# Performance work log

Hardware: AMD Instinct MI355X
Metric: run time of the kernel (lower is better)

The kernel has to match this reference:

```python
import jax, jax.numpy as jnp
import numpy as np

ITERS = 3
EPS = 1e-6


def setup_inputs() -> dict:
    key = jax.random.key(0)
    k1, k2 = jax.random.split(key, 2)
    a = jax.random.normal(k1, (64, 1152, 1, 1, 1, 1), dtype=jnp.float32)
    v = jax.random.normal(k2, (64, 1152, 32, 4, 4, 1), dtype=jnp.float32)
    logits = jnp.ones((1, 1152, 32, 1, 1, 1), dtype=jnp.float32)
    return {"a": a, "v": v, "logits": logits}


def _squash(s):
    # s: (batch, 1, B, P, P, 1); norm over dim 2 (matches torch code, dim=2)
    norm_sq = jnp.sum(s * s, axis=2, keepdims=True)
    return jnp.sqrt(norm_sq + EPS) / (1.0 + norm_sq) * s


def reference(a, v, logits):
    # a: (batch, A, 1, 1, 1, 1) -- unused (overwritten in original forward)
    # v: (batch, A, B, P, P, 1); logits: (1, A, B, 1, 1, 1)
    batch = v.shape[0]
    b = jnp.broadcast_to(logits, (batch,) + logits.shape[1:])
    p = None
    for i in range(ITERS):
        c = jax.nn.softmax(b, axis=2)                    # route over B
        s = jnp.sum(c * v, axis=1, keepdims=True)        # (batch,1,B,P,P,1)
        p = _squash(s)
        if i < ITERS - 1:
            # agreement: sum over pose dims -> (batch, A, B, 1, 1, 1)
            b = b + jnp.sum(p * v, axis=(-3, -2, -1), keepdims=True)
    p = jnp.squeeze(p, axis=1)                           # (batch, B, P, P, 1)
    a_out = jnp.linalg.norm(p, ord=2, axis=2)            # (batch, B, P, 1)
    return (a_out, p)
```

## Files before the change

kernel.cpp:

```cpp
#include <hip/hip_runtime.h>
#include <math.h>

#define BATCH 64
#define ADIM  1152
#define BDIM  32
#define SLICE 512
#define CHUNKS 16
#define ROWS  72
#define RPW   18
#define EPSQ  1e-6f
#define SPART_ITER ((size_t)BATCH * CHUNKS * SLICE)

typedef float v4f __attribute__((ext_vector_type(4)));


__device__ __forceinline__ void squash_from(const float* sp, int lane,
                                            v4f& sA, v4f& sB, v4f& fac) {
    const v4f* spv = (const v4f*)sp;
    sA = (v4f){0.f, 0.f, 0.f, 0.f};
    sB = (v4f){0.f, 0.f, 0.f, 0.f};
#pragma unroll
    for (int c = 0; c < CHUNKS; ++c) {
        sA += spv[c * 128 + lane];
        sB += spv[c * 128 + 64 + lane];
    }
    v4f nq = sA * sA + sB * sB;
#pragma unroll
    for (int off = 4; off <= 32; off <<= 1) {
        nq.x += __shfl_xor(nq.x, off, 64);
        nq.y += __shfl_xor(nq.y, off, 64);
        nq.z += __shfl_xor(nq.z, off, 64);
        nq.w += __shfl_xor(nq.w, off, 64);
    }
    fac.x = sqrtf(nq.x + EPSQ) / (1.f + nq.x);
    fac.y = sqrtf(nq.y + EPSQ) / (1.f + nq.y);
    fac.z = sqrtf(nq.z + EPSQ) / (1.f + nq.z);
    fac.w = sqrtf(nq.w + EPSQ) / (1.f + nq.w);
}

__device__ __forceinline__ void reduce_write(v4f* red, int lane, int wv,
                                             v4f ra, v4f rb, float* dst) {
    __syncthreads();
    if (wv == 3) { red[lane] = ra; red[64 + lane] = rb; }
    __syncthreads();
    if (wv == 2) { red[lane] += ra; red[64 + lane] += rb; }
    __syncthreads();
    if (wv == 1) { red[lane] += ra; red[64 + lane] += rb; }
    __syncthreads();
    if (wv == 0) {
        v4f* sp = (v4f*)dst;
        sp[lane]      = red[lane] + ra;
        sp[64 + lane] = red[64 + lane] + rb;
    }
}

__global__ __launch_bounds__(256) void pass0(
    const float* __restrict__ v,
    const float* __restrict__ logits,
    float* __restrict__ s0)
{
    const int bt    = blockIdx.x >> 4;
    const int chunk = blockIdx.x & 15;
    const int t     = threadIdx.x;
    const int lane  = t & 63;
    const int wv    = t >> 6;
    const int bq    = lane >> 2;
    const int a0    = chunk * ROWS;
    const int r0    = wv * RPW;

    __shared__ float w_sh[ROWS * BDIM];
    __shared__ v4f   red[128];

    if (t < ROWS) {
        const float* lr = logits + (size_t)(a0 + t) * BDIM;
        float e[BDIM];
        float s = 0.f;
#pragma unroll
        for (int b = 0; b < BDIM; ++b) { e[b] = __expf(lr[b]); s += e[b]; }
        float rd = 1.f / s;
#pragma unroll
        for (int b = 0; b < BDIM; ++b) w_sh[t * BDIM + b] = e[b] * rd;
    }
    __syncthreads();

    const v4f* vg = (const v4f*)(v + ((size_t)bt * ADIM + a0 + r0) * SLICE);
    v4f acc0 = (v4f){0.f, 0.f, 0.f, 0.f};
    v4f acc1 = (v4f){0.f, 0.f, 0.f, 0.f};

    v4f fA[6], fB[6];
#pragma unroll
    for (int u = 0; u < 6; ++u) fA[u] = vg[lane + 64 * u];

#pragma unroll
    for (int kk = 0; kk < 6; ++kk) {
        v4f* cur = (kk & 1) ? fB : fA;
        v4f* nxt = (kk & 1) ? fA : fB;
        if (kk + 1 < 6) {
#pragma unroll
            for (int u = 0; u < 6; ++u)
                nxt[u] = vg[lane + 64 * ((kk + 1) * 6 + u)];
        }
#pragma unroll
        for (int u = 0; u < 6; ++u) {
            const int j  = kk * 6 + u;
            const int rw = r0 + (j >> 1);
            if ((j & 1) == 0) acc0 += w_sh[rw * BDIM + bq] * cur[u];
            else              acc1 += w_sh[rw * BDIM + 16 + bq] * cur[u];
        }
    }

    reduce_write(red, lane, wv, acc0, acc1,
                 s0 + ((size_t)bt * CHUNKS + chunk) * SLICE);
}

__global__ __launch_bounds__(256) void iter_pass(
    const float* __restrict__ v,
    const float* __restrict__ logits,
    const float* __restrict__ s_part,
    float* __restrict__ s_next,
    int nprev)
{
    const int bt    = blockIdx.x >> 4;
    const int chunk = blockIdx.x & 15;
    const int t     = threadIdx.x;
    const int lane  = t & 63;
    const int wv    = t >> 6;
    const int bq    = lane >> 2;
    const int a0    = chunk * ROWS;
    const int r0    = wv * RPW;

    __shared__ v4f red[128];

    v4f pA = (v4f){0.f, 0.f, 0.f, 0.f};
    v4f pB = (v4f){0.f, 0.f, 0.f, 0.f};
    for (int j = 0; j < nprev; ++j) {
        v4f sA, sB, fac;
        squash_from(s_part + (size_t)j * SPART_ITER +
                    (size_t)bt * CHUNKS * SLICE, lane, sA, sB, fac);
        pA += fac * sA;
        pB += fac * sB;
    }

    const v4f*  vr  = (const v4f*)(v + ((size_t)bt * ADIM + a0 + r0) * SLICE);
    const float* lgr = logits + (size_t)(a0 + r0) * BDIM;

    v4f acc0 = (v4f){0.f, 0.f, 0.f, 0.f};
    v4f acc1 = (v4f){0.f, 0.f, 0.f, 0.f};

    v4f  vaN = vr[lane], vbN = vr[64 + lane];
    float b0N = lgr[bq], b1N = lgr[16 + bq];
#pragma unroll
    for (int r = 0; r < RPW; ++r) {
        v4f  va = vaN, vb = vbN;
        float b0 = b0N, b1 = b1N;
        if (r + 1 < RPW) {
            vaN = vr[(r + 1) * 128 + lane];
            vbN = vr[(r + 1) * 128 + 64 + lane];
            b0N = lgr[(r + 1) * BDIM + bq];
            b1N = lgr[(r + 1) * BDIM + 16 + bq];
        }
        float d0 = pA.x * va.x + pA.y * va.y + pA.z * va.z + pA.w * va.w;
        float d1 = pB.x * vb.x + pB.y * vb.y + pB.z * vb.z + pB.w * vb.w;
        d0 += __shfl_xor(d0, 1, 64); d0 += __shfl_xor(d0, 2, 64);
        d1 += __shfl_xor(d1, 1, 64); d1 += __shfl_xor(d1, 2, 64);
        float e0 = __expf(b0 + d0);
        float e1 = __expf(b1 + d1);
        float uu = e0 + e1;
#pragma unroll
        for (int off = 4; off <= 32; off <<= 1)
            uu += __shfl_xor(uu, off, 64);
        float rdc = __builtin_amdgcn_rcpf(uu);
        acc0 += (e0 * rdc) * va;
        acc1 += (e1 * rdc) * vb;
    }

    reduce_write(red, lane, wv, acc0, acc1,
                 s_next + ((size_t)bt * CHUNKS + chunk) * SLICE);
}

__global__ __launch_bounds__(512) void final_out(
    const float* __restrict__ s_part2,
    float* __restrict__ out)
{
    const int bt = blockIdx.x;
    const int t  = threadIdx.x;
    const int pose = t & 15;

    __shared__ float sq[SLICE];
    __shared__ float ns[16];

    float sv = 0.f;
#pragma unroll
    for (int c = 0; c < CHUNKS; ++c)
        sv += s_part2[((size_t)bt * CHUNKS + c) * SLICE + t];

    sq[t] = sv * sv;
    __syncthreads();
    if (t < 16) {
        float a = 0.f;
        for (int b2 = 0; b2 < BDIM; ++b2) a += sq[b2 * 16 + t];
        ns[t] = a;
    }
    __syncthreads();
    float n = ns[pose];
    float pv = sqrtf(n + EPSQ) / (1.f + n) * sv;

    out[8192 + (size_t)bt * SLICE + t] = pv;
    sq[t] = pv * pv;
    __syncthreads();
    if (t < 128) {
        const int b2 = t >> 2, p2 = t & 3;
        float a = 0.f;
#pragma unroll
        for (int p1 = 0; p1 < 4; ++p1) a += sq[b2 * 16 + p1 * 4 + p2];
        out[(size_t)bt * 128 + t] = sqrtf(a);
    }
}

extern "C" void kernel_launch(void* const* d_in, const int* in_sizes, int n_in,
                              void* d_out, int out_size, void* d_ws, size_t ws_size,
                              hipStream_t stream) {
    const float* v      = (const float*)d_in[1];
    const float* logits = (const float*)d_in[2];
    float* out    = (float*)d_out;
    float* s_part = (float*)d_ws;

    pass0<<<dim3(BATCH * CHUNKS), dim3(256), 0, stream>>>(
        v, logits, s_part);
    iter_pass<<<dim3(BATCH * CHUNKS), dim3(256), 0, stream>>>(
        v, logits, s_part, s_part + 1 * SPART_ITER, 1);
    iter_pass<<<dim3(BATCH * CHUNKS), dim3(256), 0, stream>>>(
        v, logits, s_part, s_part + 2 * SPART_ITER, 2);
    final_out<<<dim3(BATCH), dim3(512), 0, stream>>>(
        s_part + 2 * SPART_ITER, out);
}
```

Before: 272.2 us.

## Fuse all routing iterations into one persistent kernel with per-batch grid barriers

Replaces the four separate launches (pass0, two iter_pass, final_out) with a single kernel. Each batch's 8 chunk blocks synchronise through atomic counters in global memory, and the final squash and norm outputs are computed by chunk 0. Chunks are halved so each block covers 144 rows, and logits are cached in shared memory for reuse across iterations. This removes launch gaps and the separate final kernel. The cost is spin-wait barriers that require all 512 blocks to be co-resident to avoid deadlock, plus lower parallelism per batch.

```diff
diff --git a/kernel.cpp b/kernel.cpp
--- a/kernel.cpp
+++ b/kernel.cpp
@@ -5,9 +5,9 @@
 #define ADIM  1152
 #define BDIM  32
 #define SLICE 512
-#define CHUNKS 16
-#define ROWS  72
-#define RPW   18
+#define CHUNKS 8
+#define ROWS  144
+#define RPW   36
 #define EPSQ  1e-6f
 #define SPART_ITER ((size_t)BATCH * CHUNKS * SLICE)
 
@@ -54,13 +54,80 @@
     }
 }
 
-__global__ __launch_bounds__(256) void pass0(
+__device__ __forceinline__ void bar_release(unsigned* c) {
+    __threadfence();
+    __syncthreads();
+    if (threadIdx.x == 0)
+        __hip_atomic_fetch_add(c, 1u, __ATOMIC_RELEASE,
+                               __HIP_MEMORY_SCOPE_AGENT);
+}
+
+__device__ __forceinline__ void bar_wait(unsigned* c, unsigned target) {
+    if (threadIdx.x == 0) {
+        while (__hip_atomic_load(c, __ATOMIC_RELAXED,
+                                 __HIP_MEMORY_SCOPE_AGENT) < target)
+            __builtin_amdgcn_s_sleep(2);
+        (void)__hip_atomic_load(c, __ATOMIC_ACQUIRE,
+                                __HIP_MEMORY_SCOPE_AGENT);
+    }
+    __syncthreads();
+    __threadfence();
+}
+
+__device__ __forceinline__ void iter_sweep(const v4f* vw, const float* lg,
+                                           int lane, int bq, int r0,
+                                           v4f pA, v4f pB,
+                                           v4f& acc0, v4f& acc1) {
+    acc0 = (v4f){0.f, 0.f, 0.f, 0.f};
+    acc1 = (v4f){0.f, 0.f, 0.f, 0.f};
+    v4f fA[6], fB[6];
+#pragma unroll
+    for (int u = 0; u < 6; ++u) fA[u] = vw[lane + 64 * u];
+#pragma unroll 2
+    for (int g = 0; g < 12; ++g) {
+        v4f* cur = (g & 1) ? fB : fA;
+        v4f* nxt = (g & 1) ? fA : fB;
+        if (g + 1 < 12) {
+#pragma unroll
+            for (int u = 0; u < 6; ++u)
+                nxt[u] = vw[lane + 64 * ((g + 1) * 6 + u)];
+        }
+#pragma unroll
+        for (int i = 0; i < 3; ++i) {
+            const int rw = r0 + 3 * g + i;
+            v4f va = cur[2 * i], vb = cur[2 * i + 1];
+            float b0 = lg[rw * BDIM + bq];
+            float b1 = lg[rw * BDIM + 16 + bq];
+            float d0 = pA.x * va.x + pA.y * va.y + pA.z * va.z + pA.w * va.w;
+            float d1 = pB.x * vb.x + pB.y * vb.y + pB.z * vb.z + pB.w * vb.w;
+            d0 += __shfl_xor(d0, 1, 64); d0 += __shfl_xor(d0, 2, 64);
+            d1 += __shfl_xor(d1, 1, 64); d1 += __shfl_xor(d1, 2, 64);
+            float e0 = __expf(b0 + d0);
+            float e1 = __expf(b1 + d1);
+            float uu = e0 + e1;
+#pragma unroll
+            for (int off = 4; off <= 32; off <<= 1)
+                uu += __shfl_xor(uu, off, 64);
+            float rdc = __builtin_amdgcn_rcpf(uu);
+            acc0 += (e0 * rdc) * va;
+            acc1 += (e1 * rdc) * vb;
+        }
+    }
+}
+
+__global__ void zero_cnt(unsigned* cnt) {
+    if (threadIdx.x < BATCH) cnt[threadIdx.x] = 0u;
+}
+
+__global__ __launch_bounds__(256, 4) void route_all(
     const float* __restrict__ v,
     const float* __restrict__ logits,
-    float* __restrict__ s0)
+    float* s_part,
+    unsigned* cnt,
+    float* __restrict__ out)
 {
-    const int bt    = blockIdx.x >> 4;
-    const int chunk = blockIdx.x & 15;
+    const int bt    = blockIdx.x >> 3;
+    const int chunk = blockIdx.x & 7;
     const int t     = threadIdx.x;
     const int lane  = t & 63;
     const int wv    = t >> 6;
@@ -68,6 +135,7 @@
     const int a0    = chunk * ROWS;
     const int r0    = wv * RPW;
 
+    __shared__ float lg_sh[ROWS * BDIM];
     __shared__ float w_sh[ROWS * BDIM];
     __shared__ v4f   red[128];
 
@@ -76,144 +144,100 @@
         float e[BDIM];
         float s = 0.f;
 #pragma unroll
-        for (int b = 0; b < BDIM; ++b) { e[b] = __expf(lr[b]); s += e[b]; }
+        for (int b = 0; b < BDIM; ++b) {
+            float x = lr[b];
+            lg_sh[t * BDIM + b] = x;
+            e[b] = __expf(x);
+            s += e[b];
+        }
         float rd = 1.f / s;
 #pragma unroll
         for (int b = 0; b < BDIM; ++b) w_sh[t * BDIM + b] = e[b] * rd;
     }
     __syncthreads();
 
-    const v4f* vg = (const v4f*)(v + ((size_t)bt * ADIM + a0 + r0) * SLICE);
+    const v4f* vw = (const v4f*)(v + ((size_t)bt * ADIM + a0 + r0) * SLICE);
+    unsigned* cb = cnt + bt;
+
     v4f acc0 = (v4f){0.f, 0.f, 0.f, 0.f};
     v4f acc1 = (v4f){0.f, 0.f, 0.f, 0.f};
-
-    v4f fA[6], fB[6];
-#pragma unroll
-    for (int u = 0; u < 6; ++u) fA[u] = vg[lane + 64 * u];
-
-#pragma unroll
-    for (int kk = 0; kk < 6; ++kk) {
-        v4f* cur = (kk & 1) ? fB : fA;
-        v4f* nxt = (kk & 1) ? fA : fB;
-        if (kk + 1 < 6) {
-#pragma unroll
-            for (int u = 0; u < 6; ++u)
-                nxt[u] = vg[lane + 64 * ((kk + 1) * 6 + u)];
-        }
-#pragma unroll
-        for (int u = 0; u < 6; ++u) {
-            const int j  = kk * 6 + u;
-            const int rw = r0 + (j >> 1);
-            if ((j & 1) == 0) acc0 += w_sh[rw * BDIM + bq] * cur[u];
-            else              acc1 += w_sh[rw * BDIM + 16 + bq] * cur[u];
-        }
-    }
-
+    {
+        v4f fA[6], fB[6];
+#pragma unroll
+        for (int u = 0; u < 6; ++u) fA[u] = vw[lane + 64 * u];
+#pragma unroll 2
+        for (int kk = 0; kk < 12; ++kk) {
+            v4f* cur = (kk & 1) ? fB : fA;
+            v4f* nxt = (kk & 1) ? fA : fB;
+            if (kk + 1 < 12) {
+#pragma unroll
+                for (int u = 0; u < 6; ++u)
+                    nxt[u] = vw[lane + 64 * ((kk + 1) * 6 + u)];
+            }
+#pragma unroll
+            for (int u = 0; u < 6; ++u) {
+                const int j  = kk * 6 + u;
+                const int rw = r0 + (j >> 1);
+                if ((j & 1) == 0) acc0 += w_sh[rw * BDIM + bq] * cur[u];
+                else              acc1 += w_sh[rw * BDIM + 16 + bq] * cur[u];
+            }
+        }
+    }
     reduce_write(red, lane, wv, acc0, acc1,
-                 s0 + ((size_t)bt * CHUNKS + chunk) * SLICE);
-}
-
-__global__ __launch_bounds__(256) void iter_pass(
-    const float* __restrict__ v,
-    const float* __restrict__ logits,
-    const float* __restrict__ s_part,
-    float* __restrict__ s_next,
-    int nprev)
-{
-    const int bt    = blockIdx.x >> 4;
-    const int chunk = blockIdx.x & 15;
-    const int t     = threadIdx.x;
-    const int lane  = t & 63;
-    const int wv    = t >> 6;
-    const int bq    = lane >> 2;
-    const int a0    = chunk * ROWS;
-    const int r0    = wv * RPW;
-
-    __shared__ v4f red[128];
-
-    v4f pA = (v4f){0.f, 0.f, 0.f, 0.f};
-    v4f pB = (v4f){0.f, 0.f, 0.f, 0.f};
-    for (int j = 0; j < nprev; ++j) {
-        v4f sA, sB, fac;
-        squash_from(s_part + (size_t)j * SPART_ITER +
-                    (size_t)bt * CHUNKS * SLICE, lane, sA, sB, fac);
-        pA += fac * sA;
-        pB += fac * sB;
-    }
-
-    const v4f*  vr  = (const v4f*)(v + ((size_t)bt * ADIM + a0 + r0) * SLICE);
-    const float* lgr = logits + (size_t)(a0 + r0) * BDIM;
-
-    v4f acc0 = (v4f){0.f, 0.f, 0.f, 0.f};
-    v4f acc1 = (v4f){0.f, 0.f, 0.f, 0.f};
-
-    v4f  vaN = vr[lane], vbN = vr[64 + lane];
-    float b0N = lgr[bq], b1N = lgr[16 + bq];
-#pragma unroll
-    for (int r = 0; r < RPW; ++r) {
-        v4f  va = vaN, vb = vbN;
-        float b0 = b0N, b1 = b1N;
-        if (r + 1 < RPW) {
-            vaN = vr[(r + 1) * 128 + lane];
-            vbN = vr[(r + 1) * 128 + 64 + lane];
-            b0N = lgr[(r + 1) * BDIM + bq];
-            b1N = lgr[(r + 1) * BDIM + 16 + bq];
-        }
-        float d0 = pA.x * va.x + pA.y * va.y + pA.z * va.z + pA.w * va.w;
-        float d1 = pB.x * vb.x + pB.y * vb.y + pB.z * vb.z + pB.w * vb.w;
-        d0 += __shfl_xor(d0, 1, 64); d0 += __shfl_xor(d0, 2, 64);
-        d1 += __shfl_xor(d1, 1, 64); d1 += __shfl_xor(d1, 2, 64);
-        float e0 = __expf(b0 + d0);
-        float e1 = __expf(b1 + d1);
-        float uu = e0 + e1;
-#pragma unroll
-        for (int off = 4; off <= 32; off <<= 1)
-            uu += __shfl_xor(uu, off, 64);
-        float rdc = __builtin_amdgcn_rcpf(uu);
-        acc0 += (e0 * rdc) * va;
-        acc1 += (e1 * rdc) * vb;
-    }
-
+                 s_part + ((size_t)bt * CHUNKS + chunk) * SLICE);
+    bar_release(cb);
+    bar_wait(cb, 8);
+
+    v4f sA, sB, fac;
+    squash_from(s_part + (size_t)bt * CHUNKS * SLICE, lane, sA, sB, fac);
+    v4f pA = fac * sA;
+    v4f pB = fac * sB;
+
+    iter_sweep(vw, lg_sh, lane, bq, r0, pA, pB, acc0, acc1);
     reduce_write(red, lane, wv, acc0, acc1,
-                 s_next + ((size_t)bt * CHUNKS + chunk) * SLICE);
-}
-
-__global__ __launch_bounds__(512) void final_out(
-    const float* __restrict__ s_part2,
-    float* __restrict__ out)
-{
-    const int bt = blockIdx.x;
-    const int t  = threadIdx.x;
-    const int pose = t & 15;
-
-    __shared__ float sq[SLICE];
-    __shared__ float ns[16];
-
-    float sv = 0.f;
-#pragma unroll
-    for (int c = 0; c < CHUNKS; ++c)
-        sv += s_part2[((size_t)bt * CHUNKS + c) * SLICE + t];
-
-    sq[t] = sv * sv;
-    __syncthreads();
-    if (t < 16) {
-        float a = 0.f;
-        for (int b2 = 0; b2 < BDIM; ++b2) a += sq[b2 * 16 + t];
-        ns[t] = a;
-    }
-    __syncthreads();
-    float n = ns[pose];
-    float pv = sqrtf(n + EPSQ) / (1.f + n) * sv;
-
-    out[8192 + (size_t)bt * SLICE + t] = pv;
-    sq[t] = pv * pv;
-    __syncthreads();
-    if (t < 128) {
-        const int b2 = t >> 2, p2 = t & 3;
-        float a = 0.f;
-#pragma unroll
-        for (int p1 = 0; p1 < 4; ++p1) a += sq[b2 * 16 + p1 * 4 + p2];
-        out[(size_t)bt * 128 + t] = sqrtf(a);
+                 s_part + SPART_ITER + ((size_t)bt * CHUNKS + chunk) * SLICE);
+    bar_release(cb);
+    bar_wait(cb, 16);
+
+    squash_from(s_part + SPART_ITER + (size_t)bt * CHUNKS * SLICE,
+                lane, sA, sB, fac);
+    pA += fac * sA;
+    pB += fac * sB;
+
+    iter_sweep(vw, lg_sh, lane, bq, r0, pA, pB, acc0, acc1);
+    reduce_write(red, lane, wv, acc0, acc1,
+                 s_part + 2 * SPART_ITER + ((size_t)bt * CHUNKS + chunk) * SLICE);
+    bar_release(cb);
+
+    if (chunk != 0) return;
+    bar_wait(cb, 24);
+    if (wv != 0) return;
+
+    squash_from(s_part + 2 * SPART_ITER + (size_t)bt * CHUNKS * SLICE,
+                lane, sA, sB, fac);
+    v4f p2A = fac * sA;
+    v4f p2B = fac * sB;
+    v4f* pg = (v4f*)(out + 8192 + (size_t)bt * SLICE);
+    pg[lane]      = p2A;
+    pg[64 + lane] = p2B;
+    v4f qa = p2A * p2A;
+    v4f qb = p2B * p2B;
+#pragma unroll
+    for (int off = 1; off <= 2; off <<= 1) {
+        qa.x += __shfl_xor(qa.x, off, 64); qa.y += __shfl_xor(qa.y, off, 64);
+        qa.z += __shfl_xor(qa.z, off, 64); qa.w += __shfl_xor(qa.w, off, 64);
+        qb.x += __shfl_xor(qb.x, off, 64); qb.y += __shfl_xor(qb.y, off, 64);
+        qb.z += __shfl_xor(qb.z, off, 64); qb.w += __shfl_xor(qb.w, off, 64);
+    }
+    if ((lane & 3) == 0) {
+        v4f ra, rb;
+        ra.x = sqrtf(qa.x); ra.y = sqrtf(qa.y);
+        ra.z = sqrtf(qa.z); ra.w = sqrtf(qa.w);
+        rb.x = sqrtf(qb.x); rb.y = sqrtf(qb.y);
+        rb.z = sqrtf(qb.z); rb.w = sqrtf(qb.w);
+        v4f* ag = (v4f*)(out + (size_t)bt * 128);
+        ag[bq]      = ra;
+        ag[16 + bq] = rb;
     }
 }
 
@@ -224,13 +248,9 @@
     const float* logits = (const float*)d_in[2];
     float* out    = (float*)d_out;
     float* s_part = (float*)d_ws;
-
-    pass0<<<dim3(BATCH * CHUNKS), dim3(256), 0, stream>>>(
-        v, logits, s_part);
-    iter_pass<<<dim3(BATCH * CHUNKS), dim3(256), 0, stream>>>(
-        v, logits, s_part, s_part + 1 * SPART_ITER, 1);
-    iter_pass<<<dim3(BATCH * CHUNKS), dim3(256), 0, stream>>>(
-        v, logits, s_part, s_part + 2 * SPART_ITER, 2);
-    final_out<<<dim3(BATCH), dim3(512), 0, stream>>>(
-        s_part + 2 * SPART_ITER, out);
-}
+    unsigned* cnt = (unsigned*)((char*)d_ws + 3 * SPART_ITER * sizeof(float));
+
+    zero_cnt<<<dim3(1), dim3(64), 0, stream>>>(cnt);
+    route_all<<<dim3(BATCH * CHUNKS), dim3(256), 0, stream>>>(
+        v, logits, s_part, cnt, out);
+}
```

Result: slower. 656.9 us (+141.3%).

## Compress votes to bf16 tile in first pass and route later iterations from it

Applied to the files above, without the earlier changes.

The first routing pass now also writes a bf16 copy of v, using non-temporal fp32 loads. The two later iterations read this half-size tile instead of the fp32 input. This halves their HBM traffic, at the cost of an extra write in pass 0 and reduced precision in the agreement and weighted sums. The pass-0 reduction is also restructured to a simpler two-half LDS reduce.

```diff
diff --git a/kernel.cpp b/kernel.cpp
--- a/kernel.cpp
+++ b/kernel.cpp
@@ -4,14 +4,32 @@
 #define BATCH 64
 #define ADIM  1152
 #define BDIM  32
+#define POSE  16
 #define SLICE 512
 #define CHUNKS 16
 #define ROWS  72
 #define RPW   18
+#define WAVES 4
 #define EPSQ  1e-6f
 #define SPART_ITER ((size_t)BATCH * CHUNKS * SLICE)
 
 typedef float v4f __attribute__((ext_vector_type(4)));
+
+__device__ __forceinline__ unsigned pack_bf16x2(float a, float b) {
+    unsigned ua = __float_as_uint(a), ub = __float_as_uint(b);
+    ua = (ua + 0x7fffu + ((ua >> 16) & 1u)) >> 16;
+    ub = (ub + 0x7fffu + ((ub >> 16) & 1u));
+    return (ua & 0xffffu) | (ub & 0xffff0000u);
+}
+
+__device__ __forceinline__ v4f unpack_bf16x4(uint2 w) {
+    v4f r;
+    r.x = __uint_as_float(w.x << 16);
+    r.y = __uint_as_float(w.x & 0xffff0000u);
+    r.z = __uint_as_float(w.y << 16);
+    r.w = __uint_as_float(w.y & 0xffff0000u);
+    return r;
+}
 
 
 __device__ __forceinline__ void squash_from(const float* sp, int lane,
@@ -54,27 +72,26 @@
     }
 }
 
-__global__ __launch_bounds__(256) void pass0(
+__global__ __launch_bounds__(256) void route0_compress(
     const float* __restrict__ v,
     const float* __restrict__ logits,
-    float* __restrict__ s0)
+    uint2* __restrict__ tile,
+    float* __restrict__ s_part)
 {
     const int bt    = blockIdx.x >> 4;
     const int chunk = blockIdx.x & 15;
     const int t     = threadIdx.x;
-    const int lane  = t & 63;
-    const int wv    = t >> 6;
-    const int bq    = lane >> 2;
+    const int bc0   = (t >> 2) & 31;
+    const int hi    = t >> 7;
     const int a0    = chunk * ROWS;
-    const int r0    = wv * RPW;
 
     __shared__ float w_sh[ROWS * BDIM];
     __shared__ v4f   red[128];
 
     if (t < ROWS) {
         const float* lr = logits + (size_t)(a0 + t) * BDIM;
+        float s = 0.f;
         float e[BDIM];
-        float s = 0.f;
 #pragma unroll
         for (int b = 0; b < BDIM; ++b) { e[b] = __expf(lr[b]); s += e[b]; }
         float rd = 1.f / s;
@@ -83,13 +100,14 @@
     }
     __syncthreads();
 
-    const v4f* vg = (const v4f*)(v + ((size_t)bt * ADIM + a0 + r0) * SLICE);
-    v4f acc0 = (v4f){0.f, 0.f, 0.f, 0.f};
-    v4f acc1 = (v4f){0.f, 0.f, 0.f, 0.f};
-
+    const v4f* vg = (const v4f*)(v + ((size_t)bt * ADIM + a0) * SLICE);
+    uint2*     tg = tile + ((size_t)bt * ADIM + a0) * 128;
+
+    v4f acc = (v4f){0.f, 0.f, 0.f, 0.f};
     v4f fA[6], fB[6];
 #pragma unroll
-    for (int u = 0; u < 6; ++u) fA[u] = vg[lane + 64 * u];
+    for (int u = 0; u < 6; ++u)
+        fA[u] = __builtin_nontemporal_load(&vg[t + 256 * u]);
 
 #pragma unroll
     for (int kk = 0; kk < 6; ++kk) {
@@ -98,23 +116,31 @@
         if (kk + 1 < 6) {
 #pragma unroll
             for (int u = 0; u < 6; ++u)
-                nxt[u] = vg[lane + 64 * ((kk + 1) * 6 + u)];
+                nxt[u] = __builtin_nontemporal_load(&vg[t + 256 * ((kk + 1) * 6 + u)]);
         }
 #pragma unroll
         for (int u = 0; u < 6; ++u) {
-            const int j  = kk * 6 + u;
-            const int rw = r0 + (j >> 1);
-            if ((j & 1) == 0) acc0 += w_sh[rw * BDIM + bq] * cur[u];
-            else              acc1 += w_sh[rw * BDIM + 16 + bq] * cur[u];
-        }
-    }
-
-    reduce_write(red, lane, wv, acc0, acc1,
-                 s0 + ((size_t)bt * CHUNKS + chunk) * SLICE);
-}
-
-__global__ __launch_bounds__(256) void iter_pass(
-    const float* __restrict__ v,
+            const int k   = kk * 6 + u;
+            const int i   = t + 256 * k;
+            const int row = 2 * k + hi;
+            tg[i] = make_uint2(pack_bf16x2(cur[u].x, cur[u].y),
+                               pack_bf16x2(cur[u].z, cur[u].w));
+            float c0 = w_sh[row * BDIM + bc0];
+            acc += c0 * cur[u];
+        }
+    }
+
+    __syncthreads();
+    if (t >= 128) red[t - 128] = acc;
+    __syncthreads();
+    if (t < 128) {
+        acc += red[t];
+        ((v4f*)(s_part + ((size_t)bt * CHUNKS + chunk) * SLICE))[t] = acc;
+    }
+}
+
+__global__ __launch_bounds__(256) void iter_tile(
+    const uint2* __restrict__ tile,
     const float* __restrict__ logits,
     const float* __restrict__ s_part,
     float* __restrict__ s_next,
@@ -141,37 +167,47 @@
         pB += fac * sB;
     }
 
-    const v4f*  vr  = (const v4f*)(v + ((size_t)bt * ADIM + a0 + r0) * SLICE);
+    const uint2* tb  = tile + ((size_t)bt * ADIM + a0 + r0) * 128;
     const float* lgr = logits + (size_t)(a0 + r0) * BDIM;
 
     v4f acc0 = (v4f){0.f, 0.f, 0.f, 0.f};
     v4f acc1 = (v4f){0.f, 0.f, 0.f, 0.f};
 
-    v4f  vaN = vr[lane], vbN = vr[64 + lane];
-    float b0N = lgr[bq], b1N = lgr[16 + bq];
-#pragma unroll
-    for (int r = 0; r < RPW; ++r) {
-        v4f  va = vaN, vb = vbN;
-        float b0 = b0N, b1 = b1N;
-        if (r + 1 < RPW) {
-            vaN = vr[(r + 1) * 128 + lane];
-            vbN = vr[(r + 1) * 128 + 64 + lane];
-            b0N = lgr[(r + 1) * BDIM + bq];
-            b1N = lgr[(r + 1) * BDIM + 16 + bq];
-        }
-        float d0 = pA.x * va.x + pA.y * va.y + pA.z * va.z + pA.w * va.w;
-        float d1 = pB.x * vb.x + pB.y * vb.y + pB.z * vb.z + pB.w * vb.w;
-        d0 += __shfl_xor(d0, 1, 64); d0 += __shfl_xor(d0, 2, 64);
-        d1 += __shfl_xor(d1, 1, 64); d1 += __shfl_xor(d1, 2, 64);
-        float e0 = __expf(b0 + d0);
-        float e1 = __expf(b1 + d1);
-        float uu = e0 + e1;
-#pragma unroll
-        for (int off = 4; off <= 32; off <<= 1)
-            uu += __shfl_xor(uu, off, 64);
-        float rdc = __builtin_amdgcn_rcpf(uu);
-        acc0 += (e0 * rdc) * va;
-        acc1 += (e1 * rdc) * vb;
+    uint2 fA[6], fB[6];
+#pragma unroll
+    for (int u = 0; u < 6; ++u)
+        fA[u] = tb[(u >> 1) * 128 + (u & 1) * 64 + lane];
+
+#pragma unroll
+    for (int g = 0; g < 6; ++g) {
+        uint2* cur = (g & 1) ? fB : fA;
+        uint2* nxt = (g & 1) ? fA : fB;
+        if (g + 1 < 6) {
+#pragma unroll
+            for (int u = 0; u < 6; ++u)
+                nxt[u] = tb[(3 * (g + 1) + (u >> 1)) * 128 + (u & 1) * 64 + lane];
+        }
+#pragma unroll
+        for (int i = 0; i < 3; ++i) {
+            const int rw = 3 * g + i;
+            v4f va = unpack_bf16x4(cur[2 * i]);
+            v4f vb = unpack_bf16x4(cur[2 * i + 1]);
+            float b0 = lgr[rw * BDIM + bq];
+            float b1 = lgr[rw * BDIM + 16 + bq];
+            float d0 = pA.x * va.x + pA.y * va.y + pA.z * va.z + pA.w * va.w;
+            float d1 = pB.x * vb.x + pB.y * vb.y + pB.z * vb.z + pB.w * vb.w;
+            d0 += __shfl_xor(d0, 1, 64); d0 += __shfl_xor(d0, 2, 64);
+            d1 += __shfl_xor(d1, 1, 64); d1 += __shfl_xor(d1, 2, 64);
+            float e0 = __expf(b0 + d0);
+            float e1 = __expf(b1 + d1);
+            float uu = e0 + e1;
+#pragma unroll
+            for (int off = 4; off <= 32; off <<= 1)
+                uu += __shfl_xor(uu, off, 64);
+            float rdc = __builtin_amdgcn_rcpf(uu);
+            acc0 += (e0 * rdc) * va;
+            acc1 += (e1 * rdc) * vb;
+        }
     }
 
     reduce_write(red, lane, wv, acc0, acc1,
@@ -187,7 +223,7 @@
     const int pose = t & 15;
 
     __shared__ float sq[SLICE];
-    __shared__ float ns[16];
+    __shared__ float ns[POSE];
 
     float sv = 0.f;
 #pragma unroll
@@ -196,9 +232,9 @@
 
     sq[t] = sv * sv;
     __syncthreads();
-    if (t < 16) {
+    if (t < POSE) {
         float a = 0.f;
-        for (int b2 = 0; b2 < BDIM; ++b2) a += sq[b2 * 16 + t];
+        for (int b2 = 0; b2 < BDIM; ++b2) a += sq[b2 * POSE + t];
         ns[t] = a;
     }
     __syncthreads();
@@ -212,7 +248,7 @@
         const int b2 = t >> 2, p2 = t & 3;
         float a = 0.f;
 #pragma unroll
-        for (int p1 = 0; p1 < 4; ++p1) a += sq[b2 * 16 + p1 * 4 + p2];
+        for (int p1 = 0; p1 < 4; ++p1) a += sq[b2 * POSE + p1 * 4 + p2];
         out[(size_t)bt * 128 + t] = sqrtf(a);
     }
 }
@@ -222,15 +258,17 @@
                               hipStream_t stream) {
     const float* v      = (const float*)d_in[1];
     const float* logits = (const float*)d_in[2];
-    float* out    = (float*)d_out;
-    float* s_part = (float*)d_ws;
-
-    pass0<<<dim3(BATCH * CHUNKS), dim3(256), 0, stream>>>(
-        v, logits, s_part);
-    iter_pass<<<dim3(BATCH * CHUNKS), dim3(256), 0, stream>>>(
-        v, logits, s_part, s_part + 1 * SPART_ITER, 1);
-    iter_pass<<<dim3(BATCH * CHUNKS), dim3(256), 0, stream>>>(
-        v, logits, s_part, s_part + 2 * SPART_ITER, 2);
+    float* out = (float*)d_out;
+
+    uint2* tile   = (uint2*)d_ws;
+    float* s_part = (float*)((char*)d_ws + (size_t)BATCH * ADIM * 128 * sizeof(uint2));
+
+    route0_compress<<<dim3(BATCH * CHUNKS), dim3(256), 0, stream>>>(
+        v, logits, tile, s_part + 0 * SPART_ITER);
+    iter_tile<<<dim3(BATCH * CHUNKS), dim3(256), 0, stream>>>(
+        tile, logits, s_part, s_part + 1 * SPART_ITER, 1);
+    iter_tile<<<dim3(BATCH * CHUNKS), dim3(256), 0, stream>>>(
+        tile, logits, s_part, s_part + 2 * SPART_ITER, 2);
     final_out<<<dim3(BATCH), dim3(512), 0, stream>>>(
         s_part + 2 * SPART_ITER, out);
 }
```

Result: faster. 253.9 us (-6.7%).
